# Optimization experiments

Measured on AMD Instinct MI355X. Metric: run time of the kernel, lower is better.

## Reference

```python
import jax, jax.numpy as jnp
import numpy as np
from functools import partial

B, W, D = 512, 64, 512          # batch, window, latent_dim
H = 1024                        # hidden_dim
N, K, C = 1024, 8, 64           # codebook_size, codes_per_step, code_dim
BN = K * C                      # bottleneck dim = 512
COMMIT_W = 0.25


def setup_inputs() -> dict:
    key = jax.random.key(0)
    ks = jax.random.split(key, 16)
    s = 0.02
    return {
        "state_window": jax.random.normal(ks[0], (B, W, D), jnp.float32),
        # GRU params (PyTorch layout: [3H, in] with gate order r, z, n)
        "W_ih": jax.random.normal(ks[1], (3 * H, D), jnp.float32) * s,
        "W_hh": jax.random.normal(ks[2], (3 * H, H), jnp.float32) * s,
        "b_ih": jax.random.normal(ks[3], (3 * H,), jnp.float32) * s,
        "b_hh": jax.random.normal(ks[4], (3 * H,), jnp.float32) * s,
        # query projection
        "Wq": jax.random.normal(ks[5], (K * C, H), jnp.float32) * s,
        "bq": jnp.zeros((K * C,), jnp.float32),
        # codebook
        "emb": jax.random.normal(ks[6], (N, C), jnp.float32) * s,
        # uncertainty head: Linear(D+BN -> H), SiLU, Linear(H -> H)
        "uW1": jax.random.normal(ks[7], (H, D + BN), jnp.float32) * s,
        "ub1": jnp.zeros((H,), jnp.float32),
        "uW2": jax.random.normal(ks[8], (H, H), jnp.float32) * s,
        "ub2": jnp.zeros((H,), jnp.float32),
        # self-prediction head: Linear(BN -> H), SiLU, Linear(H -> BN)
        "pW1": jax.random.normal(ks[9], (H, BN), jnp.float32) * s,
        "pb1": jnp.zeros((H,), jnp.float32),
        "pW2": jax.random.normal(ks[10], (BN, H), jnp.float32) * s,
        "pb2": jnp.zeros((BN,), jnp.float32),
    }


def _gru(x_seq, W_ih, W_hh, b_ih, b_hh):
    """x_seq: [B, W, D] -> final hidden [B, H] (PyTorch GRU equations)."""
    # precompute input projections for all timesteps: [W, B, 3H]
    gi_all = jnp.einsum('bwd,gd->wbg', x_seq, W_ih) + b_ih

    def step(h, gi):
        gh = h @ W_hh.T + b_hh
        i_r, i_z, i_n = jnp.split(gi, 3, axis=-1)
        h_r, h_z, h_n = jnp.split(gh, 3, axis=-1)
        r = jax.nn.sigmoid(i_r + h_r)
        z = jax.nn.sigmoid(i_z + h_z)
        n = jnp.tanh(i_n + r * h_n)
        h = (1.0 - z) * n + z * h
        return h, None

    h0 = jnp.zeros((x_seq.shape[0], W_hh.shape[1]), x_seq.dtype)
    hT, _ = jax.lax.scan(step, h0, gi_all)
    return hT


def reference(state_window, W_ih, W_hh, b_ih, b_hh, Wq, bq, emb,
              uW1, ub1, uW2, ub2, pW1, pb1, pW2, pb2):
    sg = jax.lax.stop_gradient
    last_hidden = _gru(state_window, W_ih, W_hh, b_ih, b_hh)      # [B, H]

    queries = (last_hidden @ Wq.T + bq).reshape(-1, K, C)          # [B, K, C]

    # VQ: pairwise squared distances to codebook [B, K, N]
    d = (jnp.sum(queries ** 2, axis=-1, keepdims=True)
         + jnp.sum(emb ** 2, axis=-1)[None, None, :]
         - 2.0 * jnp.einsum('bkc,nc->bkn', queries, emb))
    code_indices = jnp.argmin(d, axis=-1)                          # [B, K] int
    quantized = emb[code_indices]                                  # [B, K, C]

    commit_loss = jnp.mean((sg(queries) - quantized) ** 2)
    codebook_loss = jnp.mean((queries - sg(quantized)) ** 2)
    vq_loss = codebook_loss + COMMIT_W * commit_loss
    quantized_st = queries + sg(quantized - queries)               # straight-through

    narrator_state = quantized_st.reshape(quantized_st.shape[0], -1)  # [B, K*C]
    last_world_state = state_window[:, -1]                            # [B, D]

    u_in = jnp.concatenate([last_world_state, narrator_state], axis=-1)
    uncertainty = jax.nn.silu(u_in @ uW1.T + ub1) @ uW2.T + ub2       # [B, H]
    predicted_next_state = jax.nn.silu(narrator_state @ pW1.T + pb1) @ pW2.T + pb2  # [B, K*C]

    return (code_indices, quantized_st, narrator_state, uncertainty,
            predicted_next_state, vq_loss, last_hidden)
```

## Files before the change

kernel.cpp:

```cpp
#include <hip/hip_runtime.h>
#include <math.h>

#define B_ 512
#define W_ 64
#define D_ 512
#define H_ 1024
#define NC_ 1024
#define K_ 8
#define C_ 64
#define BN_ 512
#define G3 (3*H_)

typedef unsigned short u16;
typedef __attribute__((ext_vector_type(8))) short bf16x8;
typedef __attribute__((ext_vector_type(4))) float f32x4;

__device__ __forceinline__ float bf_up(u16 h) { return __uint_as_float(((unsigned)h) << 16); }
__device__ __forceinline__ u16 bf_rn(float x) {
    unsigned u = __float_as_uint(x);
    return (u16)((u + 0x7FFFu + ((u >> 16) & 1u)) >> 16);
}

__device__ __forceinline__ void split8v(float4 x, float4 y, uint4& H, uint4& L) {
    float v[8] = {x.x, x.y, x.z, x.w, y.x, y.y, y.z, y.w};
    union { u16 s[8]; uint4 u; } Hh, Ll;
    #pragma unroll
    for (int i = 0; i < 8; ++i) {
        unsigned ub = __float_as_uint(v[i]);
        u16 hi = (u16)(ub >> 16);
        Hh.s[i] = hi;
        Ll.s[i] = bf_rn(v[i] - bf_up(hi));
    }
    H = Hh.u; L = Ll.u;
}

__device__ __forceinline__ void cvt_store8(u16* ph, u16* pl, float4 x, float4 y) {
    uint4 H, L; split8v(x, y, H, L);
    *(uint4*)ph = H;
    *(uint4*)pl = L;
}

struct GArgs {
    const float* A;  long lda;
    const float* Bw;
    const u16* Bhi;  const u16* Blo;
    const float* bias;
    float* C;  long ldc;
    int K;
};

template<int ACT, int BPRE>
__device__ __forceinline__ void gemm_core64(const GArgs g, int bx, int by, u16* lds)
{
    u16* Ah = lds;
    u16* Al = lds + 2560;
    u16* Bh = lds + 5120;
    u16* Bl = lds + 7680;
    const int tid = threadIdx.x;
    const int l = tid & 63, wv = tid >> 6;
    const int m0 = by * 64, n0 = bx * 64;
    const int sr = tid >> 2, sc = (tid & 3) * 8;
    const int sA = sr * 40 + sc;

    const float* Ap = g.A + (long)(m0 + sr) * g.lda + sc;
    const float* Bp = 0; const u16 *Bph = 0, *Bpl = 0;
    if (BPRE) { Bph = g.Bhi + (long)(n0 + sr) * g.K + sc; Bpl = g.Blo + (long)(n0 + sr) * g.K + sc; }
    else      { Bp  = g.Bw  + (long)(n0 + sr) * g.K + sc; }

    f32x4 acc[4] = {};

    for (int k0 = 0; k0 < g.K; k0 += 32) {
        float4 a0 = *(const float4*)(Ap + k0);
        float4 a1 = *(const float4*)(Ap + k0 + 4);
        float4 b0, b1; uint4 h0, l0;
        if (BPRE) { h0 = *(const uint4*)(Bph + k0); l0 = *(const uint4*)(Bpl + k0); }
        else      { b0 = *(const float4*)(Bp + k0); b1 = *(const float4*)(Bp + k0 + 4); }
        __syncthreads();
        cvt_store8(Ah + sA, Al + sA, a0, a1);
        if (BPRE) { *(uint4*)(Bh + sA) = h0; *(uint4*)(Bl + sA) = l0; }
        else      { cvt_store8(Bh + sA, Bl + sA, b0, b1); }
        __syncthreads();

        const int fr = (l & 15) * 40 + (l >> 4) * 8;
        bf16x8 bh = *(const bf16x8*)(Bh + wv * 640 + fr);
        bf16x8 bl = *(const bf16x8*)(Bl + wv * 640 + fr);
        #pragma unroll
        for (int mt = 0; mt < 4; ++mt) {
            bf16x8 ah = *(const bf16x8*)(Ah + mt * 640 + fr);
            bf16x8 al = *(const bf16x8*)(Al + mt * 640 + fr);
            acc[mt] = __builtin_amdgcn_mfma_f32_16x16x32_bf16(ah, bh, acc[mt], 0, 0, 0);
            acc[mt] = __builtin_amdgcn_mfma_f32_16x16x32_bf16(ah, bl, acc[mt], 0, 0, 0);
            acc[mt] = __builtin_amdgcn_mfma_f32_16x16x32_bf16(al, bh, acc[mt], 0, 0, 0);
        }
    }

    const int n = n0 + wv * 16 + (l & 15);
    const float bv = g.bias[n];
    #pragma unroll
    for (int mt = 0; mt < 4; ++mt) {
        #pragma unroll
        for (int r = 0; r < 4; ++r) {
            int m = m0 + mt * 16 + (l >> 4) * 4 + r;
            float v = acc[mt][r] + bv;
            if (ACT == 1) v = v / (1.f + expf(-v));
            g.C[(long)m * g.ldc + n] = v;
        }
    }
}

template<int ACT, int BPRE>
__global__ __launch_bounds__(256)
void hilo_gemm64(GArgs g) {
    __shared__ u16 lds[10240];
    gemm_core64<ACT, BPRE>(g, blockIdx.x, blockIdx.y, lds);
}

struct FS6 {
    const u16* hFh_in; const u16* hFl_in;
    u16* hFh_out; u16* hFl_out;
    float* h_f32_out;
    const u16* WFh; const u16* WFl;
    const u16* XWh; const u16* XWl;
    const u16* xFh; const u16* xFl;
    const float* b_hh; const float* b_ih;
};

__global__ __launch_bounds__(256)
void gru_step7(FS6 f)
{
    __shared__ u16 lds[16384];
    const int tid = threadIdx.x, l = tid & 63, wv = tid >> 6;
    const int mh = wv & 1, nh = wv >> 1;
    const int by = blockIdx.x >> 5, bx = blockIdx.x & 31;

    const int t0 = tid >> 6;
    const int mf0 = t0 & 1, pl0 = t0 >> 1;
    const u16* giP0 = (pl0 ? f.xFl : f.xFh) + (long)(by * 2 + mf0) * (16 * 512) + (long)l * 8;
    const u16* ghP0 = (pl0 ? f.hFl_in : f.hFh_in) + (long)(by * 2 + mf0) * (32 * 512) + (long)l * 8;
    const int lo0 = pl0 * 1024 + (mf0 * 64 + l) * 8;

    #define MKB_(c2, giP, ghP, lo) \
        { int lane_ = (c2) & 63, t_ = (c2) >> 6; int nf_ = t_ % 6, pl_ = t_ / 6; \
          giP = (pl_ ? f.XWl : f.XWh) + (long)(bx * 6 + nf_) * (16 * 512) + (long)lane_ * 8; \
          ghP = (pl_ ? f.WFl : f.WFh) + (long)(bx * 6 + nf_) * (32 * 512) + (long)lane_ * 8; \
          lo = 2048 + pl_ * 3072 + (nf_ * 64 + lane_) * 8; }
    const u16 *giP1, *ghP1, *giP2, *ghP2, *giP3, *ghP3;
    int lo1, lo2, lo3;
    MKB_(tid,       giP1, ghP1, lo1);
    MKB_(tid + 256, giP2, ghP2, lo2);
    MKB_(tid + 512, giP3, ghP3, lo3);
    #undef MKB_

    f32x4 gi0 = {}, gi1 = {}, gi2 = {}, gh0 = {}, gh1 = {}, gh2 = {};

    #define LDR7(st, R0, R1, R2, R3) { \
        if ((st) >= 16) { long ko = (long)((st) - 16) * 512; \
            R0 = *(const uint4*)(ghP0 + ko); R1 = *(const uint4*)(ghP1 + ko); \
            R2 = *(const uint4*)(ghP2 + ko); R3 = *(const uint4*)(ghP3 + ko); } \
        else { long ko = (long)(st) * 512; \
            R0 = *(const uint4*)(giP0 + ko); R1 = *(const uint4*)(giP1 + ko); \
            R2 = *(const uint4*)(giP2 + ko); R3 = *(const uint4*)(giP3 + ko); } }

    #define WRL7(bi, R0, R1, R2, R3) { u16* bb_ = lds + (bi) * 8192; \
        *(uint4*)(bb_ + lo0) = R0; *(uint4*)(bb_ + lo1) = R1; \
        *(uint4*)(bb_ + lo2) = R2; *(uint4*)(bb_ + lo3) = R3; }

    #define CMP7(st) { \
        const u16* bb_ = lds + ((st) & 1) * 8192; \
        bf16x8 ah  = *(const bf16x8*)(bb_ + (mh * 64 + l) * 8); \
        bf16x8 al  = *(const bf16x8*)(bb_ + 1024 + (mh * 64 + l) * 8); \
        bf16x8 b0h = *(const bf16x8*)(bb_ + 2048 + ((nh * 3 + 0) * 64 + l) * 8); \
        bf16x8 b1h = *(const bf16x8*)(bb_ + 2048 + ((nh * 3 + 1) * 64 + l) * 8); \
        bf16x8 b2h = *(const bf16x8*)(bb_ + 2048 + ((nh * 3 + 2) * 64 + l) * 8); \
        bf16x8 b0l = *(const bf16x8*)(bb_ + 5120 + ((nh * 3 + 0) * 64 + l) * 8); \
        bf16x8 b1l = *(const bf16x8*)(bb_ + 5120 + ((nh * 3 + 1) * 64 + l) * 8); \
        bf16x8 b2l = *(const bf16x8*)(bb_ + 5120 + ((nh * 3 + 2) * 64 + l) * 8); \
        if ((st) < 16) { \
            gi0 = __builtin_amdgcn_mfma_f32_16x16x32_bf16(ah, b0h, gi0, 0, 0, 0); \
            gi0 = __builtin_amdgcn_mfma_f32_16x16x32_bf16(ah, b0l, gi0, 0, 0, 0); \
            gi0 = __builtin_amdgcn_mfma_f32_16x16x32_bf16(al, b0h, gi0, 0, 0, 0); \
            gi1 = __builtin_amdgcn_mfma_f32_16x16x32_bf16(ah, b1h, gi1, 0, 0, 0); \
            gi1 = __builtin_amdgcn_mfma_f32_16x16x32_bf16(ah, b1l, gi1, 0, 0, 0); \
            gi1 = __builtin_amdgcn_mfma_f32_16x16x32_bf16(al, b1h, gi1, 0, 0, 0); \
            gi2 = __builtin_amdgcn_mfma_f32_16x16x32_bf16(ah, b2h, gi2, 0, 0, 0); \
            gi2 = __builtin_amdgcn_mfma_f32_16x16x32_bf16(ah, b2l, gi2, 0, 0, 0); \
            gi2 = __builtin_amdgcn_mfma_f32_16x16x32_bf16(al, b2h, gi2, 0, 0, 0); \
        } else { \
            gh0 = __builtin_amdgcn_mfma_f32_16x16x32_bf16(ah, b0h, gh0, 0, 0, 0); \
            gh0 = __builtin_amdgcn_mfma_f32_16x16x32_bf16(ah, b0l, gh0, 0, 0, 0); \
            gh0 = __builtin_amdgcn_mfma_f32_16x16x32_bf16(al, b0h, gh0, 0, 0, 0); \
            gh1 = __builtin_amdgcn_mfma_f32_16x16x32_bf16(ah, b1h, gh1, 0, 0, 0); \
            gh1 = __builtin_amdgcn_mfma_f32_16x16x32_bf16(ah, b1l, gh1, 0, 0, 0); \
            gh1 = __builtin_amdgcn_mfma_f32_16x16x32_bf16(al, b1h, gh1, 0, 0, 0); \
            gh2 = __builtin_amdgcn_mfma_f32_16x16x32_bf16(ah, b2h, gh2, 0, 0, 0); \
            gh2 = __builtin_amdgcn_mfma_f32_16x16x32_bf16(ah, b2l, gh2, 0, 0, 0); \
            gh2 = __builtin_amdgcn_mfma_f32_16x16x32_bf16(al, b2h, gh2, 0, 0, 0); \
        } }

    uint4 a0, a1, a2, a3, b0, b1, b2, b3;
    LDR7(0, a0, a1, a2, a3); WRL7(0, a0, a1, a2, a3);
    LDR7(1, a0, a1, a2, a3);
    LDR7(2, b0, b1, b2, b3);
    __syncthreads();
    #pragma unroll
    for (int s2 = 0; s2 < 48; s2 += 2) {
        CMP7(s2);
        if (s2 + 1 < 48) WRL7(1, a0, a1, a2, a3);
        if (s2 + 3 < 48) LDR7(s2 + 3, a0, a1, a2, a3);
        __syncthreads();
        CMP7(s2 + 1);
        if (s2 + 2 < 48) WRL7(0, b0, b1, b2, b3);
        if (s2 + 4 < 48) LDR7(s2 + 4, b0, b1, b2, b3);
        __syncthreads();
    }
    #undef LDR7
    #undef WRL7
    #undef CMP7

    const int mfG = by * 2 + mh;
    const int j = (bx * 2 + nh) * 16 + (l & 15);
    const float bir = f.b_ih[j], biz = f.b_ih[H_ + j], bin2 = f.b_ih[2 * H_ + j];
    const float bhr = f.b_hh[j], bhz = f.b_hh[H_ + j], bhn = f.b_hh[2 * H_ + j];
    const int kcj = j >> 5, laneTop = ((j >> 3) & 3) * 16, sj = j & 7;
    const long foB = ((long)(mfG * 32 + kcj) * 64) * 8 + sj;
    const bool wf32 = (f.h_f32_out != nullptr);
    #pragma unroll
    for (int r = 0; r < 4; ++r) {
        int mlow = (l >> 4) * 4 + r;
        long fo = foB + (long)(mlow + laneTop) * 8;
        float hprev = bf_up(f.hFh_in[fo]) + bf_up(f.hFl_in[fo]);
        float ir = gi0[r] + bir, iz = gi1[r] + biz, inn = gi2[r] + bin2;
        float hr = gh0[r] + bhr, hz = gh1[r] + bhz, hn = gh2[r] + bhn;
        float rg = 1.f / (1.f + expf(-(ir + hr)));
        float zg = 1.f / (1.f + expf(-(iz + hz)));
        float ng = tanhf(inn + rg * hn);
        float hv = (1.f - zg) * ng + zg * hprev;
        unsigned ub = __float_as_uint(hv);
        u16 hh = (u16)(ub >> 16);
        f.hFh_out[fo] = hh;
        f.hFl_out[fo] = bf_rn(hv - bf_up(hh));
        if (wf32) {
            int m = by * 32 + mh * 16 + mlow;
            f.h_f32_out[(long)m * H_ + j] = hv;
        }
    }
}

__global__ __launch_bounds__(256)
void to_hilo(const float* __restrict__ src, u16* __restrict__ hi, u16* __restrict__ lo, long n8) {
    long i = (long)blockIdx.x * 256 + threadIdx.x;
    if (i >= n8) return;
    float4 a = ((const float4*)src)[2 * i];
    float4 b = ((const float4*)src)[2 * i + 1];
    uint4 H, L; split8v(a, b, H, L);
    ((uint4*)hi)[i] = H;
    ((uint4*)lo)[i] = L;
}

template<int KD, int NKC>
__global__ __launch_bounds__(256)
void prep_w48(const float* __restrict__ W, u16* __restrict__ fh, u16* __restrict__ fl)
{
    long t = (long)blockIdx.x * 256 + threadIdx.x;
    if (t >= (long)192 * NKC * 64) return;
    int l = (int)(t & 63);
    long nk = t >> 6;
    int kc = (int)(nk % NKC);
    int nf = (int)(nk / NKC);
    int p = nf * 16 + (l & 15);
    int jg = p / 48, g = (p % 48) >> 4, jl = p & 15;
    int srow = g * H_ + jg * 16 + jl;
    int k0 = kc * 32 + (l >> 4) * 8;
    float4 v0 = *(const float4*)(W + (long)srow * KD + k0);
    float4 v1 = *(const float4*)(W + (long)srow * KD + k0 + 4);
    uint4 H, L; split8v(v0, v1, H, L);
    ((uint4*)fh)[t] = H;
    ((uint4*)fl)[t] = L;
}

__global__ __launch_bounds__(256)
void pack_x_all(const float* __restrict__ x, u16* __restrict__ dh, u16* __restrict__ dl)
{
    #pragma unroll
    for (int it = 0; it < 4; ++it) {
        long e4 = (long)blockIdx.x * 1024 + it * 256 + threadIdx.x;
        int b  = (int)(e4 >> 13);
        int rem = (int)(e4 & 8191);
        int w  = rem >> 7;
        int dd = (rem & 127) * 4;
        float4 v = *(const float4*)(x + (long)b * (W_ * D_) + (long)w * D_ + dd);
        union { u16 s[4]; uint2 u; } Hh, Ll;
        float vv[4] = {v.x, v.y, v.z, v.w};
        #pragma unroll
        for (int i = 0; i < 4; ++i) {
            unsigned ub = __float_as_uint(vv[i]);
            u16 hi = (u16)(ub >> 16);
            Hh.s[i] = hi;
            Ll.s[i] = bf_rn(vv[i] - bf_up(hi));
        }
        int mf = b >> 4, kc = dd >> 5;
        int lane = (b & 15) + ((dd >> 3) & 3) * 16;
        long fo = (long)w * 262144 + ((long)(mf * 16 + kc) * 64 + lane) * 8 + (dd & 7);
        *(uint2*)(dh + fo) = Hh.u;
        *(uint2*)(dl + fo) = Ll.u;
    }
}

struct StepArgs {
    const float* h_in;  float* h_out;
    const float* W_hh;
    const float* gi;
    const float* b_hh;
    const float* xw;
    const float* W_ih;
    const float* b_ih;
    float* gi_out;
};

__global__ __launch_bounds__(256)
void gru_step2(StepArgs s)
{
    __shared__ u16 lds[17920];
    const int id = blockIdx.x;
    const int tid = threadIdx.x;
    if (id >= 256) {
        if (!s.xw) return;
        int id2 = id - 256;
        GArgs g;
        g.A = s.xw; g.lda = (long)W_ * D_;
        g.Bw = s.W_ih; g.Bhi = 0; g.Blo = 0;
        g.bias = s.b_ih; g.C = s.gi_out; g.ldc = G3; g.K = D_;
        gemm_core64<0, 0>(g, id2 % 48, id2 / 48, lds);
        return;
    }
    u16* Ah = lds;
    u16* Al = lds + 1280;
    u16* Bh = lds + 2560;
    u16* Bl = lds + 10240;
    const int by = id >> 4, bx = id & 15;
    const int l = tid & 63, wv = tid >> 6;
    const int m0 = by * 32, j0 = bx * 64;
    const int sr = tid >> 2, sc = (tid & 3) * 8;
    const int sA = sr * 40 + sc;

    const float* Ap = s.h_in + (long)(m0 + (tid >> 2)) * H_ + sc;

    f32x4 acc[2][3] = {};

    for (int k0 = 0; k0 < H_; k0 += 32) {
        float4 a0, a1;
        if (tid < 128) {
            a0 = *(const float4*)(Ap + k0);
            a1 = *(const float4*)(Ap + k0 + 4);
        }
        float4 bf0[3], bf1[3];
        #pragma unroll
        for (int g = 0; g < 3; ++g) {
            long rowp = (long)(g * H_ + j0 + sr);
            bf0[g] = *(const float4*)(s.W_hh + rowp * H_ + k0 + sc);
            bf1[g] = *(const float4*)(s.W_hh + rowp * H_ + k0 + sc + 4);
        }
        __syncthreads();
        if (tid < 128) cvt_store8(Ah + sA, Al + sA, a0, a1);
        #pragma unroll
        for (int g = 0; g < 3; ++g)
            cvt_store8(Bh + g * 2560 + sA, Bl + g * 2560 + sA, bf0[g], bf1[g]);
        __syncthreads();

        const int fr = (l & 15) * 40 + (l >> 4) * 8;
        bf16x8 bhf[3], blf[3];
        #pragma unroll
        for (int g = 0; g < 3; ++g) {
            bhf[g] = *(const bf16x8*)(Bh + g * 2560 + wv * 640 + fr);
            blf[g] = *(const bf16x8*)(Bl + g * 2560 + wv * 640 + fr);
        }
        #pragma unroll
        for (int mt = 0; mt < 2; ++mt) {
            bf16x8 ah = *(const bf16x8*)(Ah + mt * 640 + fr);
            bf16x8 al = *(const bf16x8*)(Al + mt * 640 + fr);
            #pragma unroll
            for (int g = 0; g < 3; ++g) {
                acc[mt][g] = __builtin_amdgcn_mfma_f32_16x16x32_bf16(ah, bhf[g], acc[mt][g], 0, 0, 0);
                acc[mt][g] = __builtin_amdgcn_mfma_f32_16x16x32_bf16(ah, blf[g], acc[mt][g], 0, 0, 0);
                acc[mt][g] = __builtin_amdgcn_mfma_f32_16x16x32_bf16(al, bhf[g], acc[mt][g], 0, 0, 0);
            }
        }
    }

    const int j = j0 + wv * 16 + (l & 15);
    const float bhr = s.b_hh[j], bhz = s.b_hh[H_ + j], bhn = s.b_hh[2 * H_ + j];
    #pragma unroll
    for (int mt = 0; mt < 2; ++mt) {
        #pragma unroll
        for (int r = 0; r < 4; ++r) {
            int m = m0 + mt * 16 + (l >> 4) * 4 + r;
            const float* gib = s.gi + (long)m * G3;
            float ir = gib[j], iz = gib[H_ + j], inn = gib[2 * H_ + j];
            float hr = acc[mt][0][r] + bhr;
            float hz = acc[mt][1][r] + bhz;
            float hn = acc[mt][2][r] + bhn;
            float rg = 1.f / (1.f + expf(-(ir + hr)));
            float zg = 1.f / (1.f + expf(-(iz + hz)));
            float ng = tanhf(inn + rg * hn);
            s.h_out[(long)m * H_ + j] = (1.f - zg) * ng + zg * s.h_in[(long)m * H_ + j];
        }
    }
}

__global__ void emb_norm(const float* __restrict__ emb, float* __restrict__ e2,
                         float* __restrict__ loss_slot)
{
    int n = blockIdx.x * 256 + threadIdx.x;
    if (n == 0) *loss_slot = 0.f;
    if (n < NC_) {
        const float4* e4 = (const float4*)(emb + (long)n * C_);
        float s = 0.f;
        #pragma unroll
        for (int c = 0; c < 16; ++c) { float4 e = e4[c]; s += e.x*e.x + e.y*e.y + e.z*e.z + e.w*e.w; }
        e2[n] = s;
    }
}

__global__ __launch_bounds__(256)
void vq16(const float* __restrict__ q, const float* __restrict__ emb,
          const float* __restrict__ e2, float* __restrict__ out_f,
          int* __restrict__ out_i)
{
    __shared__ float es[128 * 68];
    const int blk = blockIdx.x, tid = threadIdx.x;
    const int qg = tid >> 4, sI = tid & 15;
    float4 qr[16];
    {
        const float4* qrow = (const float4*)(q + (long)(blk * 16 + qg) * C_);
        #pragma unroll
        for (int i = 0; i < 16; ++i) qr[i] = qrow[i];
    }
    float bestv = 3.4e38f; int besti = 0;

    for (int n0 = 0; n0 < NC_; n0 += 128) {
        __syncthreads();
        const float4* e4 = (const float4*)(emb + (long)n0 * C_);
        #pragma unroll
        for (int i = tid; i < 2048; i += 256) {
            int code = i >> 4, c4 = i & 15;
            *(float4*)(es + code * 68 + c4 * 4) = e4[i];
        }
        __syncthreads();
        #pragma unroll
        for (int jj = 0; jj < 8; ++jj) {
            int code = sI + 16 * jj;
            const float* er = es + code * 68;
            float dot = 0.f;
            #pragma unroll
            for (int c4 = 0; c4 < 16; ++c4) {
                float4 ev = *(const float4*)(er + c4 * 4);
                dot += ev.x * qr[c4].x + ev.y * qr[c4].y + ev.z * qr[c4].z + ev.w * qr[c4].w;
            }
            float d = e2[n0 + code] - 2.f * dot;
            if (d < bestv) { bestv = d; besti = n0 + code; }
        }
    }
    #pragma unroll
    for (int m = 1; m <= 8; m <<= 1) {
        float ov = __shfl_xor(bestv, m);
        int   oi = __shfl_xor(besti, m);
        if (ov < bestv || (ov == bestv && oi < besti)) { bestv = ov; besti = oi; }
    }
    if (sI == 0) {
        int bk = blk * 16 + qg;
        out_f[bk] = (float)besti;
        out_i[bk] = besti;
    }
}

__global__ __launch_bounds__(256)
void gather_loss(const float* __restrict__ q, const float* __restrict__ emb,
                 const int* __restrict__ idx, float* __restrict__ quant_out,
                 float* __restrict__ narr_out, float* __restrict__ loss_slot)
{
    int i = blockIdx.x * 256 + threadIdx.x;
    int bk = i >> 6;
    int c  = i & 63;
    float e  = emb[(long)idx[bk] * C_ + c];
    float qv = q[i];
    quant_out[i] = e;
    narr_out[i]  = e;
    float dsq = (qv - e) * (qv - e);
    __shared__ float red[256];
    red[threadIdx.x] = dsq;
    __syncthreads();
    for (int s = 128; s > 0; s >>= 1) {
        if (threadIdx.x < s) red[threadIdx.x] += red[threadIdx.x + s];
        __syncthreads();
    }
    if (threadIdx.x == 0)
        atomicAdd(loss_slot, red[0] * (1.25f / (float)(B_ * K_ * C_)));
}

__global__ __launch_bounds__(256)
void build_uin(const float* __restrict__ x, const float* __restrict__ narr,
               float* __restrict__ uin)
{
    int i = blockIdx.x * 256 + threadIdx.x;
    int b = i >> 10;
    int j = i & 1023;
    uin[i] = (j < D_) ? x[(long)b * W_ * D_ + (long)(W_ - 1) * D_ + j]
                      : narr[(long)b * BN_ + (j - D_)];
}

__global__ __launch_bounds__(256)
void copy_f(const float* __restrict__ src, float* __restrict__ dst)
{
    int i = blockIdx.x * 256 + threadIdx.x;
    dst[i] = src[i];
}

extern "C" void kernel_launch(void* const* d_in, const int* in_sizes, int n_in,
                              void* d_out, int out_size, void* d_ws, size_t ws_size,
                              hipStream_t stream)
{
    (void)in_sizes; (void)n_in; (void)out_size;
    const float* x     = (const float*)d_in[0];
    const float* W_ih  = (const float*)d_in[1];
    const float* W_hh  = (const float*)d_in[2];
    const float* b_ih  = (const float*)d_in[3];
    const float* b_hh  = (const float*)d_in[4];
    const float* Wq    = (const float*)d_in[5];
    const float* bq    = (const float*)d_in[6];
    const float* emb   = (const float*)d_in[7];
    const float* uW1   = (const float*)d_in[8];
    const float* ub1   = (const float*)d_in[9];
    const float* uW2   = (const float*)d_in[10];
    const float* ub2   = (const float*)d_in[11];
    const float* pW1   = (const float*)d_in[12];
    const float* pb1   = (const float*)d_in[13];
    const float* pW2   = (const float*)d_in[14];
    const float* pb2   = (const float*)d_in[15];

    float* ws = (float*)d_ws;
    float* hA   = ws;
    float* giA  = ws + 524288;
    float* giB  = ws + 2097152;
    float* q    = ws + 3670016;
    float* e2   = ws + 3932160;
    int*   idxi = (int*)(ws + 3933184);
    const long FLOAT_WORDS = 3937280;
    float* uin  = giB;
    float* mlph = giB + 524288;
    float* t1   = giA;

    u16* wsu = (u16*)((char*)d_ws + FLOAT_WORDS * sizeof(float));
    u16* whhF_h = wsu;             u16* whhF_l = wsu + 3145728;
    u16* wihF_h = wsu + 6291456;   u16* wihF_l = wsu + 7864320;
    u16* wqR_h  = wsu + 9437184;   u16* wqR_l  = wsu + 9961472;
    u16* uw1R_h = wsu + 10485760;  u16* uw1R_l = wsu + 11534336;
    u16* uw2R_h = wsu + 12582912;  u16* uw2R_l = wsu + 13631488;
    u16* pw1R_h = wsu + 14680064;  u16* pw1R_l = wsu + 15204352;
    u16* pw2R_h = wsu + 15728640;  u16* pw2R_l = wsu + 16252928;
    u16* hF_h[2] = { wsu + 16777216, wsu + 17301504 };
    u16* hF_l[2] = { wsu + 17825792, wsu + 18350080 };
    u16* xF_h = wsu + 18874368;
    u16* xF_l = wsu + 35651584;
    const size_t NEED_NEW = FLOAT_WORDS * sizeof(float) + (size_t)52428800 * 2;
    const bool fast = ws_size >= NEED_NEW;

    float* out = (float*)d_out;
    const long o_idx   = 0;
    const long o_quant = o_idx   + (long)B_ * K_;
    const long o_narr  = o_quant + (long)B_ * K_ * C_;
    const long o_unc   = o_narr  + (long)B_ * BN_;
    const long o_pred  = o_unc   + (long)B_ * H_;
    const long o_loss  = o_pred  + (long)B_ * BN_;
    const long o_lh    = o_loss  + 1;

    float* hB = out + o_unc;
    float* hbuf[2] = { hA, hB };
    float* gibuf[2] = { giA, giB };

    hipMemsetAsync(hA, 0, (size_t)B_ * H_ * sizeof(float), stream);
    emb_norm<<<4, 256, 0, stream>>>(emb, e2, out + o_loss);

    auto mkargs = [&](const float* A, long lda, const float* Bw, const u16* Bh, const u16* Bl,
                      const float* bias, float* C, long ldc, int Kd) {
        GArgs g; g.A = A; g.lda = lda; g.Bw = Bw; g.Bhi = Bh; g.Blo = Bl;
        g.bias = bias; g.C = C; g.ldc = ldc; g.K = Kd; return g;
    };
    auto cvt = [&](const float* s, u16* hi, u16* lo, long n) {
        long n8 = n / 8;
        to_hilo<<<(int)((n8 + 255) / 256), 256, 0, stream>>>(s, hi, lo, n8);
    };

    if (fast) {
        hipMemsetAsync(hF_h[0], 0, (size_t)B_ * H_ * sizeof(u16), stream);
        hipMemsetAsync(hF_l[0], 0, (size_t)B_ * H_ * sizeof(u16), stream);
        prep_w48<H_, 32><<<1536, 256, 0, stream>>>(W_hh, whhF_h, whhF_l);
        prep_w48<D_, 16><<<768, 256, 0, stream>>>(W_ih, wihF_h, wihF_l);
        cvt(Wq,  wqR_h,  wqR_l,  (long)BN_ * H_);
        cvt(uW1, uw1R_h, uw1R_l, (long)H_ * (D_ + BN_));
        cvt(uW2, uw2R_h, uw2R_l, (long)H_ * H_);
        cvt(pW1, pw1R_h, pw1R_l, (long)H_ * BN_);
        cvt(pW2, pw2R_h, pw2R_l, (long)BN_ * H_);
        pack_x_all<<<4096, 256, 0, stream>>>(x, xF_h, xF_l);

        for (int w = 0; w < W_; ++w) {
            FS6 f;
            f.hFh_in = hF_h[w & 1];        f.hFl_in = hF_l[w & 1];
            f.hFh_out = hF_h[(w + 1) & 1]; f.hFl_out = hF_l[(w + 1) & 1];
            f.h_f32_out = (w == W_ - 1) ? hA : nullptr;
            f.WFh = whhF_h; f.WFl = whhF_l;
            f.XWh = wihF_h; f.XWl = wihF_l;
            f.xFh = xF_h + (long)w * 262144;
            f.xFl = xF_l + (long)w * 262144;
            f.b_hh = b_hh; f.b_ih = b_ih;
            gru_step7<<<512, 256, 0, stream>>>(f);
        }

        auto gemm = [&](int act, GArgs g, int N, int M) {
            dim3 grid(N / 64, M / 64);
            if (act == 1) hilo_gemm64<1, 1><<<grid, 256, 0, stream>>>(g);
            else          hilo_gemm64<0, 1><<<grid, 256, 0, stream>>>(g);
        };
        gemm(0, mkargs(hA, H_, Wq, wqR_h, wqR_l, bq, q, BN_, H_), BN_, B_);
        vq16<<<256, 256, 0, stream>>>(q, emb, e2, out + o_idx, idxi);
        gather_loss<<<(B_ * K_ * C_) / 256, 256, 0, stream>>>(
            q, emb, idxi, out + o_quant, out + o_narr, out + o_loss);
        build_uin<<<(B_ * (D_ + BN_)) / 256, 256, 0, stream>>>(x, out + o_narr, uin);
        gemm(1, mkargs(uin, D_ + BN_, uW1, uw1R_h, uw1R_l, ub1, mlph, H_, D_ + BN_), H_, B_);
        gemm(0, mkargs(mlph, H_, uW2, uw2R_h, uw2R_l, ub2, out + o_unc, H_, H_), H_, B_);
        gemm(1, mkargs(out + o_narr, BN_, pW1, pw1R_h, pw1R_l, pb1, t1, H_, BN_), H_, B_);
        gemm(0, mkargs(t1, H_, pW2, pw2R_h, pw2R_l, pb2, out + o_pred, BN_, H_), BN_, B_);
        copy_f<<<(B_ * H_) / 256, 256, 0, stream>>>(hA, out + o_lh);
        return;
    }

    {
        GArgs g0 = mkargs(x, (long)W_ * D_, W_ih, 0, 0, b_ih, gibuf[0], G3, D_);
        hilo_gemm64<0, 0><<<dim3(48, 8), 256, 0, stream>>>(g0);
    }
    for (int w = 0; w < W_; ++w) {
        StepArgs s;
        s.h_in  = hbuf[w & 1];
        s.h_out = hbuf[(w + 1) & 1];
        s.W_hh = W_hh;
        s.gi = gibuf[w & 1];
        s.b_hh = b_hh;
        s.xw = (w + 1 < W_) ? (x + (long)(w + 1) * D_) : nullptr;
        s.W_ih = W_ih;
        s.b_ih = b_ih;
        s.gi_out = gibuf[(w + 1) & 1];
        gru_step2<<<640, 256, 0, stream>>>(s);
    }
    float* hfin = hbuf[0];

    auto gemmL = [&](int act, GArgs g, int N, int M) {
        dim3 grid(N / 64, M / 64);
        if (act == 1) hilo_gemm64<1, 0><<<grid, 256, 0, stream>>>(g);
        else          hilo_gemm64<0, 0><<<grid, 256, 0, stream>>>(g);
    };
    gemmL(0, mkargs(hfin, H_, Wq, 0, 0, bq, q, BN_, H_), BN_, B_);
    vq16<<<256, 256, 0, stream>>>(q, emb, e2, out + o_idx, idxi);
    gather_loss<<<(B_ * K_ * C_) / 256, 256, 0, stream>>>(
        q, emb, idxi, out + o_quant, out + o_narr, out + o_loss);
    build_uin<<<(B_ * (D_ + BN_)) / 256, 256, 0, stream>>>(x, out + o_narr, uin);
    gemmL(1, mkargs(uin, D_ + BN_, uW1, 0, 0, ub1, mlph, H_, D_ + BN_), H_, B_);
    gemmL(0, mkargs(mlph, H_, uW2, 0, 0, ub2, out + o_unc, H_, H_), H_, B_);
    gemmL(1, mkargs(out + o_narr, BN_, pW1, 0, 0, pb1, t1, H_, BN_), H_, B_);
    gemmL(0, mkargs(t1, H_, pW2, 0, 0, pb2, out + o_pred, BN_, H_), BN_, B_);
    copy_f<<<(B_ * H_) / 256, 256, 0, stream>>>(hfin, out + o_lh);
}
```

Before: 1.691 ms.

## Load GRU weight fragments straight to registers and vectorise x packing

The GRU step kernel now reads each wave's weight (B operand) fragments straight from global memory into registers, double-buffered in registers. Only the shared hidden/input (A) tiles still go through LDS, which shrinks LDS from 32KB to 8KB and removes the LDS round trip for the weights. This uses more VGPRs for the prefetched fragments, which could lower occupancy. The x packing kernel also now handles 8 elements per thread with 128-bit stores, using the existing split helper, and launches half as many blocks.

```diff
diff --git a/kernel.cpp b/kernel.cpp
--- a/kernel.cpp
+++ b/kernel.cpp
@@ -126,9 +126,9 @@
 };
 
 __global__ __launch_bounds__(256)
-void gru_step7(FS6 f)
-{
-    __shared__ u16 lds[16384];
+void gru_step9(FS6 f)
+{
+    __shared__ u16 lds[4096];
     const int tid = threadIdx.x, l = tid & 63, wv = tid >> 6;
     const int mh = wv & 1, nh = wv >> 1;
     const int by = blockIdx.x >> 5, bx = blockIdx.x & 31;
@@ -139,83 +139,86 @@
     const u16* ghP0 = (pl0 ? f.hFl_in : f.hFh_in) + (long)(by * 2 + mf0) * (32 * 512) + (long)l * 8;
     const int lo0 = pl0 * 1024 + (mf0 * 64 + l) * 8;
 
-    #define MKB_(c2, giP, ghP, lo) \
-        { int lane_ = (c2) & 63, t_ = (c2) >> 6; int nf_ = t_ % 6, pl_ = t_ / 6; \
-          giP = (pl_ ? f.XWl : f.XWh) + (long)(bx * 6 + nf_) * (16 * 512) + (long)lane_ * 8; \
-          ghP = (pl_ ? f.WFl : f.WFh) + (long)(bx * 6 + nf_) * (32 * 512) + (long)lane_ * 8; \
-          lo = 2048 + pl_ * 3072 + (nf_ * 64 + lane_) * 8; }
-    const u16 *giP1, *ghP1, *giP2, *ghP2, *giP3, *ghP3;
-    int lo1, lo2, lo3;
-    MKB_(tid,       giP1, ghP1, lo1);
-    MKB_(tid + 256, giP2, ghP2, lo2);
-    MKB_(tid + 512, giP3, ghP3, lo3);
-    #undef MKB_
+    const long nfb = (long)(bx * 6 + nh * 3);
+    const u16* bGIh = f.XWh + nfb * 8192 + (long)l * 8;
+    const u16* bGIl = f.XWl + nfb * 8192 + (long)l * 8;
+    const u16* bGHh = f.WFh + nfb * 16384 + (long)l * 8;
+    const u16* bGHl = f.WFl + nfb * 16384 + (long)l * 8;
 
     f32x4 gi0 = {}, gi1 = {}, gi2 = {}, gh0 = {}, gh1 = {}, gh2 = {};
 
-    #define LDR7(st, R0, R1, R2, R3) { \
+    #define LDRA9(st, R) { \
+        if ((st) >= 16) R = *(const uint4*)(ghP0 + (long)((st) - 16) * 512); \
+        else            R = *(const uint4*)(giP0 + (long)(st) * 512); }
+
+    #define WRLA9(bi, R) { *(uint4*)(lds + (bi) * 2048 + lo0) = R; }
+
+    #define LDRB9(st, B0h, B1h, B2h, B0l, B1l, B2l) { \
         if ((st) >= 16) { long ko = (long)((st) - 16) * 512; \
-            R0 = *(const uint4*)(ghP0 + ko); R1 = *(const uint4*)(ghP1 + ko); \
-            R2 = *(const uint4*)(ghP2 + ko); R3 = *(const uint4*)(ghP3 + ko); } \
-        else { long ko = (long)(st) * 512; \
-            R0 = *(const uint4*)(giP0 + ko); R1 = *(const uint4*)(giP1 + ko); \
-            R2 = *(const uint4*)(giP2 + ko); R3 = *(const uint4*)(giP3 + ko); } }
-
-    #define WRL7(bi, R0, R1, R2, R3) { u16* bb_ = lds + (bi) * 8192; \
-        *(uint4*)(bb_ + lo0) = R0; *(uint4*)(bb_ + lo1) = R1; \
-        *(uint4*)(bb_ + lo2) = R2; *(uint4*)(bb_ + lo3) = R3; }
-
-    #define CMP7(st) { \
-        const u16* bb_ = lds + ((st) & 1) * 8192; \
-        bf16x8 ah  = *(const bf16x8*)(bb_ + (mh * 64 + l) * 8); \
-        bf16x8 al  = *(const bf16x8*)(bb_ + 1024 + (mh * 64 + l) * 8); \
-        bf16x8 b0h = *(const bf16x8*)(bb_ + 2048 + ((nh * 3 + 0) * 64 + l) * 8); \
-        bf16x8 b1h = *(const bf16x8*)(bb_ + 2048 + ((nh * 3 + 1) * 64 + l) * 8); \
-        bf16x8 b2h = *(const bf16x8*)(bb_ + 2048 + ((nh * 3 + 2) * 64 + l) * 8); \
-        bf16x8 b0l = *(const bf16x8*)(bb_ + 5120 + ((nh * 3 + 0) * 64 + l) * 8); \
-        bf16x8 b1l = *(const bf16x8*)(bb_ + 5120 + ((nh * 3 + 1) * 64 + l) * 8); \
-        bf16x8 b2l = *(const bf16x8*)(bb_ + 5120 + ((nh * 3 + 2) * 64 + l) * 8); \
+            B0h = *(const uint4*)(bGHh + ko);          B1h = *(const uint4*)(bGHh + 16384 + ko); \
+            B2h = *(const uint4*)(bGHh + 32768 + ko); \
+            B0l = *(const uint4*)(bGHl + ko);          B1l = *(const uint4*)(bGHl + 16384 + ko); \
+            B2l = *(const uint4*)(bGHl + 32768 + ko); \
+        } else { long ko = (long)(st) * 512; \
+            B0h = *(const uint4*)(bGIh + ko);          B1h = *(const uint4*)(bGIh + 8192 + ko); \
+            B2h = *(const uint4*)(bGIh + 16384 + ko); \
+            B0l = *(const uint4*)(bGIl + ko);          B1l = *(const uint4*)(bGIl + 8192 + ko); \
+            B2l = *(const uint4*)(bGIl + 16384 + ko); } }
+
+    #define CMP9(st, B0h, B1h, B2h, B0l, B1l, B2l) { \
+        const u16* bb_ = lds + ((st) & 1) * 2048; \
+        bf16x8 ah = *(const bf16x8*)(bb_ + (mh * 64 + l) * 8); \
+        bf16x8 al = *(const bf16x8*)(bb_ + 1024 + (mh * 64 + l) * 8); \
+        bf16x8 c0h = *(const bf16x8*)&B0h; bf16x8 c1h = *(const bf16x8*)&B1h; bf16x8 c2h = *(const bf16x8*)&B2h; \
+        bf16x8 c0l = *(const bf16x8*)&B0l; bf16x8 c1l = *(const bf16x8*)&B1l; bf16x8 c2l = *(const bf16x8*)&B2l; \
         if ((st) < 16) { \
-            gi0 = __builtin_amdgcn_mfma_f32_16x16x32_bf16(ah, b0h, gi0, 0, 0, 0); \
-            gi0 = __builtin_amdgcn_mfma_f32_16x16x32_bf16(ah, b0l, gi0, 0, 0, 0); \
-            gi0 = __builtin_amdgcn_mfma_f32_16x16x32_bf16(al, b0h, gi0, 0, 0, 0); \
-            gi1 = __builtin_amdgcn_mfma_f32_16x16x32_bf16(ah, b1h, gi1, 0, 0, 0); \
-            gi1 = __builtin_amdgcn_mfma_f32_16x16x32_bf16(ah, b1l, gi1, 0, 0, 0); \
-            gi1 = __builtin_amdgcn_mfma_f32_16x16x32_bf16(al, b1h, gi1, 0, 0, 0); \
-            gi2 = __builtin_amdgcn_mfma_f32_16x16x32_bf16(ah, b2h, gi2, 0, 0, 0); \
-            gi2 = __builtin_amdgcn_mfma_f32_16x16x32_bf16(ah, b2l, gi2, 0, 0, 0); \
-            gi2 = __builtin_amdgcn_mfma_f32_16x16x32_bf16(al, b2h, gi2, 0, 0, 0); \
+            gi0 = __builtin_amdgcn_mfma_f32_16x16x32_bf16(ah, c0h, gi0, 0, 0, 0); \
+            gi0 = __builtin_amdgcn_mfma_f32_16x16x32_bf16(ah, c0l, gi0, 0, 0, 0); \
+            gi0 = __builtin_amdgcn_mfma_f32_16x16x32_bf16(al, c0h, gi0, 0, 0, 0); \
+            gi1 = __builtin_amdgcn_mfma_f32_16x16x32_bf16(ah, c1h, gi1, 0, 0, 0); \
+            gi1 = __builtin_amdgcn_mfma_f32_16x16x32_bf16(ah, c1l, gi1, 0, 0, 0); \
+            gi1 = __builtin_amdgcn_mfma_f32_16x16x32_bf16(al, c1h, gi1, 0, 0, 0); \
+            gi2 = __builtin_amdgcn_mfma_f32_16x16x32_bf16(ah, c2h, gi2, 0, 0, 0); \
+            gi2 = __builtin_amdgcn_mfma_f32_16x16x32_bf16(ah, c2l, gi2, 0, 0, 0); \
+            gi2 = __builtin_amdgcn_mfma_f32_16x16x32_bf16(al, c2h, gi2, 0, 0, 0); \
         } else { \
-            gh0 = __builtin_amdgcn_mfma_f32_16x16x32_bf16(ah, b0h, gh0, 0, 0, 0); \
-            gh0 = __builtin_amdgcn_mfma_f32_16x16x32_bf16(ah, b0l, gh0, 0, 0, 0); \
-            gh0 = __builtin_amdgcn_mfma_f32_16x16x32_bf16(al, b0h, gh0, 0, 0, 0); \
-            gh1 = __builtin_amdgcn_mfma_f32_16x16x32_bf16(ah, b1h, gh1, 0, 0, 0); \
-            gh1 = __builtin_amdgcn_mfma_f32_16x16x32_bf16(ah, b1l, gh1, 0, 0, 0); \
-            gh1 = __builtin_amdgcn_mfma_f32_16x16x32_bf16(al, b1h, gh1, 0, 0, 0); \
-            gh2 = __builtin_amdgcn_mfma_f32_16x16x32_bf16(ah, b2h, gh2, 0, 0, 0); \
-            gh2 = __builtin_amdgcn_mfma_f32_16x16x32_bf16(ah, b2l, gh2, 0, 0, 0); \
-            gh2 = __builtin_amdgcn_mfma_f32_16x16x32_bf16(al, b2h, gh2, 0, 0, 0); \
+            gh0 = __builtin_amdgcn_mfma_f32_16x16x32_bf16(ah, c0h, gh0, 0, 0, 0); \
+            gh0 = __builtin_amdgcn_mfma_f32_16x16x32_bf16(ah, c0l, gh0, 0, 0, 0); \
+            gh0 = __builtin_amdgcn_mfma_f32_16x16x32_bf16(al, c0h, gh0, 0, 0, 0); \
+            gh1 = __builtin_amdgcn_mfma_f32_16x16x32_bf16(ah, c1h, gh1, 0, 0, 0); \
+            gh1 = __builtin_amdgcn_mfma_f32_16x16x32_bf16(ah, c1l, gh1, 0, 0, 0); \
+            gh1 = __builtin_amdgcn_mfma_f32_16x16x32_bf16(al, c1h, gh1, 0, 0, 0); \
+            gh2 = __builtin_amdgcn_mfma_f32_16x16x32_bf16(ah, c2h, gh2, 0, 0, 0); \
+            gh2 = __builtin_amdgcn_mfma_f32_16x16x32_bf16(ah, c2l, gh2, 0, 0, 0); \
+            gh2 = __builtin_amdgcn_mfma_f32_16x16x32_bf16(al, c2h, gh2, 0, 0, 0); \
         } }
 
-    uint4 a0, a1, a2, a3, b0, b1, b2, b3;
-    LDR7(0, a0, a1, a2, a3); WRL7(0, a0, a1, a2, a3);
-    LDR7(1, a0, a1, a2, a3);
-    LDR7(2, b0, b1, b2, b3);
+    uint4 a0, b0;
+    uint4 sB0h, sB1h, sB2h, sB0l, sB1l, sB2l;
+    uint4 tB0h, tB1h, tB2h, tB0l, tB1l, tB2l;
+    LDRA9(0, a0); WRLA9(0, a0);
+    LDRA9(1, a0);
+    LDRA9(2, b0);
+    LDRB9(0, sB0h, sB1h, sB2h, sB0l, sB1l, sB2l);
+    LDRB9(1, tB0h, tB1h, tB2h, tB0l, tB1l, tB2l);
     __syncthreads();
     #pragma unroll
     for (int s2 = 0; s2 < 48; s2 += 2) {
-        CMP7(s2);
-        if (s2 + 1 < 48) WRL7(1, a0, a1, a2, a3);
-        if (s2 + 3 < 48) LDR7(s2 + 3, a0, a1, a2, a3);
-        __syncthreads();
-        CMP7(s2 + 1);
-        if (s2 + 2 < 48) WRL7(0, b0, b1, b2, b3);
-        if (s2 + 4 < 48) LDR7(s2 + 4, b0, b1, b2, b3);
-        __syncthreads();
-    }
-    #undef LDR7
-    #undef WRL7
-    #undef CMP7
+        CMP9(s2, sB0h, sB1h, sB2h, sB0l, sB1l, sB2l);
+        WRLA9(1, a0);
+        if (s2 + 3 < 48) LDRA9(s2 + 3, a0);
+        if (s2 + 2 < 48) LDRB9(s2 + 2, sB0h, sB1h, sB2h, sB0l, sB1l, sB2l);
+        __syncthreads();
+        CMP9(s2 + 1, tB0h, tB1h, tB2h, tB0l, tB1l, tB2l);
+        if (s2 + 2 < 48) WRLA9(0, b0);
+        if (s2 + 4 < 48) LDRA9(s2 + 4, b0);
+        if (s2 + 3 < 48) LDRB9(s2 + 3, tB0h, tB1h, tB2h, tB0l, tB1l, tB2l);
+        __syncthreads();
+    }
+    #undef LDRA9
+    #undef WRLA9
+    #undef LDRB9
+    #undef CMP9
 
     const int mfG = by * 2 + mh;
     const int j = (bx * 2 + nh) * 16 + (l & 15);
@@ -281,28 +284,22 @@
 __global__ __launch_bounds__(256)
 void pack_x_all(const float* __restrict__ x, u16* __restrict__ dh, u16* __restrict__ dl)
 {
+    const int tid = threadIdx.x;
+    const int lane_lo = tid & 15, sel = (tid >> 4) & 3;
     #pragma unroll
     for (int it = 0; it < 4; ++it) {
-        long e4 = (long)blockIdx.x * 1024 + it * 256 + threadIdx.x;
-        int b  = (int)(e4 >> 13);
-        int rem = (int)(e4 & 8191);
-        int w  = rem >> 7;
-        int dd = (rem & 127) * 4;
-        float4 v = *(const float4*)(x + (long)b * (W_ * D_) + (long)w * D_ + dd);
-        union { u16 s[4]; uint2 u; } Hh, Ll;
-        float vv[4] = {v.x, v.y, v.z, v.w};
-        #pragma unroll
-        for (int i = 0; i < 4; ++i) {
-            unsigned ub = __float_as_uint(vv[i]);
-            u16 hi = (u16)(ub >> 16);
-            Hh.s[i] = hi;
-            Ll.s[i] = bf_rn(vv[i] - bf_up(hi));
-        }
-        int mf = b >> 4, kc = dd >> 5;
-        int lane = (b & 15) + ((dd >> 3) & 3) * 16;
-        long fo = (long)w * 262144 + ((long)(mf * 16 + kc) * 64 + lane) * 8 + (dd & 7);
-        *(uint2*)(dh + fo) = Hh.u;
-        *(uint2*)(dl + fo) = Ll.u;
+        int g = blockIdx.x * 16 + it * 4 + (tid >> 6);
+        int mf = g & 31, kc = (g >> 5) & 15, w = g >> 9;
+        int b = mf * 16 + lane_lo;
+        int dd = kc * 32 + sel * 8;
+        int lane = lane_lo + sel * 16;
+        const float* src = x + (long)b * (W_ * D_) + (long)w * D_ + dd;
+        float4 v0 = *(const float4*)src;
+        float4 v1 = *(const float4*)(src + 4);
+        uint4 H, L; split8v(v0, v1, H, L);
+        long fo = (long)w * 262144 + ((long)(mf * 16 + kc) * 64 + lane) * 8;
+        *(uint4*)(dh + fo) = H;
+        *(uint4*)(dl + fo) = L;
     }
 }
 
@@ -600,7 +597,7 @@
         cvt(uW2, uw2R_h, uw2R_l, (long)H_ * H_);
         cvt(pW1, pw1R_h, pw1R_l, (long)H_ * BN_);
         cvt(pW2, pw2R_h, pw2R_l, (long)BN_ * H_);
-        pack_x_all<<<4096, 256, 0, stream>>>(x, xF_h, xF_l);
+        pack_x_all<<<2048, 256, 0, stream>>>(x, xF_h, xF_l);
 
         for (int w = 0; w < W_; ++w) {
             FS6 f;
@@ -612,7 +609,7 @@
             f.xFh = xF_h + (long)w * 262144;
             f.xFl = xF_l + (long)w * 262144;
             f.b_hh = b_hh; f.b_ih = b_ih;
-            gru_step7<<<512, 256, 0, stream>>>(f);
+            gru_step9<<<512, 256, 0, stream>>>(f);
         }
 
         auto gemm = [&](int act, GArgs g, int N, int M) {
```

Result: slower. 1.808 ms (+7.0%).
